# Kernel optimization log

Hardware: AMD Instinct MI355X
Metric: run time of the kernel (lower is better)

## Reference

```python
import math
import jax, jax.numpy as jnp
import numpy as np

NUM_HEADS, RAD_PTS, LVL_PTS = 8, 4, 1
P = RAD_PTS * LVL_PTS


def setup_inputs() -> dict:
    B, Nq, Din = 2, 21760, 256
    hw = np.array([[128, 128], [64, 64], [32, 32], [16, 16]], np.int64)
    sizes = hw[:, 0] * hw[:, 1]
    offs = np.concatenate([[0], np.cumsum(sizes)[:-1]]).astype(np.int64)
    Ns = int(sizes.sum())
    map_ids = np.tile(np.repeat(np.arange(4), sizes)[None], (B, 1)).astype(np.int64)

    key = jax.random.key(0)
    ks = jax.random.split(key, 8)
    in_feats = jax.random.normal(ks[0], (B, Nq, Din), jnp.float32)
    sample_feats = jax.random.normal(ks[1], (B, Ns, Din), jnp.float32)
    sample_priors = jax.random.uniform(ks[2], (B, Nq, 2), jnp.float32)

    # sample_offsets bias: radial grid init as in the torch module
    thetas = np.arange(NUM_HEADS) * (2.0 * math.pi / NUM_HEADS)
    grid = np.stack([np.cos(thetas), np.sin(thetas), np.zeros(NUM_HEADS)], 1)
    grid = grid / np.abs(grid).max(1, keepdims=True)
    grid = np.tile(grid.reshape(NUM_HEADS, 1, 1, 3), (1, RAD_PTS, LVL_PTS, 1))
    grid = grid * np.arange(1, RAD_PTS + 1).reshape(1, RAD_PTS, 1, 1)
    bo = jnp.asarray(grid.reshape(-1), jnp.float32)

    Wo = jax.random.normal(ks[3], (NUM_HEADS * P * 3, Din), jnp.float32) * 0.01
    Wa = jax.random.normal(ks[4], (NUM_HEADS * P, Din), jnp.float32) * 0.01
    ba = jnp.zeros((NUM_HEADS * P,), jnp.float32)
    s = 1.0 / np.sqrt(Din)
    Wv = jax.random.normal(ks[5], (Din, Din), jnp.float32) * s
    bv = jnp.zeros((Din,), jnp.float32)
    Wout = jax.random.normal(ks[6], (Din, Din), jnp.float32) * s
    bout = jnp.zeros((Din,), jnp.float32)

    return dict(in_feats=in_feats, sample_priors=sample_priors, sample_feats=sample_feats,
                map_hw=jnp.asarray(hw), map_offs=jnp.asarray(offs), map_ids=jnp.asarray(map_ids),
                Wo=Wo, bo=bo, Wa=Wa, ba=ba, Wv=Wv, bv=bv, Wout=Wout, bout=bout)


def _trilinear_sample(val, map_hw, map_offs, xy, z, L):
    # val [B,Ns,H,D]; xy [B,Q,H,P,2] normalized; z [B,Q,H,P] in ~[0,1]
    B, Ns, H, D = val.shape
    Q = xy.shape[1]
    val_t = val.transpose(0, 2, 1, 3)  # [B,H,Ns,D]
    x, y = xy[..., 0], xy[..., 1]
    lvl_f = z * (L - 1)
    l0 = jnp.floor(lvl_f).astype(jnp.int32)
    wz = lvl_f - l0.astype(lvl_f.dtype)

    def gather(idx):  # idx [B,Q,H,P] int32 -> [B,Q,H,P,D]
        it = idx.transpose(0, 2, 1, 3).reshape(B, H, Q * P, 1)
        g = jnp.take_along_axis(val_t, it, axis=2)  # [B,H,Q*P,D]
        return g.reshape(B, H, Q, P, D).transpose(0, 2, 1, 3, 4)

    def sample_level(lvl):  # bilinear sample within pyramid level `lvl` (zero padding)
        valid_l = (lvl >= 0) & (lvl < L)
        lc = jnp.clip(lvl, 0, L - 1)
        Hl = map_hw[lc, 0].astype(jnp.int32)
        Wl = map_hw[lc, 1].astype(jnp.int32)
        off = map_offs[lc].astype(jnp.int32)
        xf = x * Wl.astype(x.dtype) - 0.5
        yf = y * Hl.astype(x.dtype) - 0.5
        x0 = jnp.floor(xf).astype(jnp.int32)
        y0 = jnp.floor(yf).astype(jnp.int32)
        dx = xf - x0.astype(x.dtype)
        dy = yf - y0.astype(x.dtype)
        out = jnp.zeros((B, Q, H, P, D), x.dtype)
        corners = [(x0, y0, (1 - dx) * (1 - dy)), (x0 + 1, y0, dx * (1 - dy)),
                   (x0, y0 + 1, (1 - dx) * dy), (x0 + 1, y0 + 1, dx * dy)]
        for xi, yi, w in corners:
            ok = valid_l & (xi >= 0) & (xi < Wl) & (yi >= 0) & (yi < Hl)
            idx = off + jnp.clip(yi, 0, Hl - 1) * Wl + jnp.clip(xi, 0, Wl - 1)
            out = out + gather(idx) * (w * ok.astype(x.dtype))[..., None]
        return out

    return sample_level(l0) * (1 - wz)[..., None] + sample_level(l0 + 1) * wz[..., None]


def reference(in_feats, sample_priors, sample_feats, map_hw, map_offs, map_ids,
              Wo, bo, Wa, ba, Wv, bv, Wout, bout):
    B, Nq, _ = in_feats.shape
    Ns = sample_feats.shape[1]
    L = map_hw.shape[0]
    D = Wv.shape[0] // NUM_HEADS

    val = (sample_feats @ Wv.T + bv).reshape(B, Ns, NUM_HEADS, D)
    offs = (in_feats @ Wo.T + bo).reshape(B, Nq, NUM_HEADS, P, 3)

    # sample_priors last dim == 2: normalize offsets by (W, H) of the query's map
    norm = map_hw[:, ::-1][map_ids].astype(offs.dtype)  # [B,Nq,2] (w,h)
    sample_xy = sample_priors[:, :, None, None, :2] + offs[..., :2] / norm[:, :, None, None, :]

    lvl_off = jnp.arange(LVL_PTS, dtype=offs.dtype) - 0.5 * (LVL_PTS - 1)
    z_grid = map_ids[:, :, None, None, None].astype(offs.dtype) + lvl_off  # [B,Nq,1,1,Lp]
    z_grid = jnp.broadcast_to(z_grid, (B, Nq, NUM_HEADS, RAD_PTS, LVL_PTS)).reshape(B, Nq, NUM_HEADS, P)
    sample_z = (z_grid + jnp.tanh(offs[..., 2])) / (L - 1)

    attn = jax.nn.softmax((in_feats @ Wa.T + ba).reshape(B, Nq, NUM_HEADS, P), axis=3)

    sampled = _trilinear_sample(val, map_hw, map_offs, sample_xy, sample_z, L)  # [B,Nq,H,P,D]
    attn_feats = jnp.einsum('bqhpd,bqhp->bqhd', sampled, attn).reshape(B, Nq, NUM_HEADS * D)
    return attn_feats @ Wout.T + bout
```

## Files before the change

### kernel.cpp

```cpp
#include <hip/hip_runtime.h>
#include <hip/hip_bf16.h>
#include <math.h>

typedef __bf16 bf16x8 __attribute__((ext_vector_type(8)));
typedef float f32x4 __attribute__((ext_vector_type(4)));
typedef float f32x2 __attribute__((ext_vector_type(2)));
typedef unsigned short ushort8 __attribute__((ext_vector_type(8)));

static __device__ __forceinline__ unsigned short f2bf(float f) {
    union { float f; unsigned u; } c; c.f = f;
    unsigned r = c.u + 0x7FFFu + ((c.u >> 16) & 1u);
    return (unsigned short)(r >> 16);
}

static __device__ __forceinline__ void gload_lds16(
    const unsigned short* g, unsigned short* l)
{
    __builtin_amdgcn_global_load_lds(
        (const __attribute__((address_space(1))) void*)g,
        (__attribute__((address_space(3))) void*)l, 16, 0, 0);
}

__global__ __launch_bounds__(256) void convert_weights_hist(
    const float* __restrict__ Wv, const float* __restrict__ Wo,
    const float* __restrict__ Wa, const float* __restrict__ Wout,
    const float* __restrict__ bo, const float* __restrict__ ba,
    unsigned short* __restrict__ Wv_b, unsigned short* __restrict__ Woa_b,
    unsigned short* __restrict__ Wout_b, float* __restrict__ boa,
    const float* __restrict__ priors, int* __restrict__ counts,
    int BQ, int Nq)
{
    __shared__ int cnt[16];
    if (threadIdx.x < 16) cnt[threadIdx.x] = 0;
    __syncthreads();

    int gid = blockIdx.x * blockDim.x + threadIdx.x;
    int stride = gridDim.x * blockDim.x;
    for (int i = gid; i < 163840; i += stride) {
        if (i < 65536)       Wv_b[i] = f2bf(Wv[i]);
        else if (i < 90112)  Woa_b[i - 65536] = f2bf(Wo[i - 65536]);
        else if (i < 98304)  Woa_b[i - 65536] = f2bf(Wa[i - 90112]);
        else                 Wout_b[i - 98304] = f2bf(Wout[i - 98304]);
    }
    if (gid < 96)       boa[gid] = bo[gid];
    else if (gid < 128) boa[gid] = ba[gid - 96];

    for (int q = gid; q < BQ; q += stride) {
        int b = q / Nq;
        float py = priors[(size_t)q * 2 + 1];
        int band = min(7, max(0, (int)(py * 8.0f)));
        atomicAdd(&cnt[b * 8 + band], 1);
    }
    __syncthreads();
    if (threadIdx.x < 16 && cnt[threadIdx.x] > 0)
        atomicAdd(&counts[threadIdx.x], cnt[threadIdx.x]);
}

__global__ __launch_bounds__(256) void bucket_scatter(
    const float* __restrict__ priors, const int* __restrict__ counts,
    int* __restrict__ cursors, int* __restrict__ qidx, int BQ, int Nq)
{
    __shared__ int lcnt[16];
    __shared__ int lbase[16];
    const int tid = threadIdx.x;
    if (tid < 16) lcnt[tid] = 0;
    __syncthreads();
    int q = blockIdx.x * 256 + tid;
    int mybucket = 0, myslot = 0;
    bool valid = q < BQ;
    if (valid) {
        int b = q / Nq;
        float py = priors[(size_t)q * 2 + 1];
        int band = min(7, max(0, (int)(py * 8.0f)));
        mybucket = b * 8 + band;
        myslot = atomicAdd(&lcnt[mybucket], 1);
    }
    __syncthreads();
    if (tid < 16) {
        int base = 0;
        #pragma unroll
        for (int i = 0; i < 16; ++i) base += (i < tid) ? counts[i] : 0;
        lbase[tid] = base + atomicAdd(&cursors[tid], lcnt[tid]);
    }
    __syncthreads();
    if (valid) qidx[lbase[mybucket] + myslot] = q;
}

template<int WN, bool A_BF16, int OUT_MODE>
__global__ __launch_bounds__(WN * 64) void gemm_mfma(
    const void* __restrict__ Av, const unsigned short* __restrict__ W,
    const float* __restrict__ bias, void* __restrict__ Cv,
    int M, int N, int K, int NsPB)
{
    constexpr int BM = 64;
    constexpr int BN = WN * 64;
    constexpr int BK = 64;
    constexpr int NTHR = WN * 64;
    constexpr int LDP = 72;
    constexpr int ASZ = A_BF16 ? (BM * 64) : (BM * LDP);

    __shared__ __align__(16) unsigned short As[ASZ];
    __shared__ __align__(16) unsigned short Bs[BN * 64];

    const int bm  = blockIdx.x * BM;
    const int bn  = blockIdx.y * BN;
    const int tid = threadIdx.x;
    const int wid = tid >> 6;
    const int lane = tid & 63;
    const int lr = lane & 15;
    const int lg = lane >> 4;
    const int lrow = lane >> 3;
    const int lc16 = (lane & 7) ^ (lrow & 7);

    f32x4 acc[4][4];
    #pragma unroll
    for (int mi = 0; mi < 4; ++mi)
        #pragma unroll
        for (int ni = 0; ni < 4; ++ni)
            acc[mi][ni] = (f32x4){0.f, 0.f, 0.f, 0.f};

    for (int kt = 0; kt < K; kt += BK) {
        #pragma unroll
        for (int c = wid; c < BN / 8; c += WN) {
            const unsigned short* g =
                W + (size_t)(bn + c * 8 + lrow) * K + kt + lc16 * 8;
            gload_lds16(g, Bs + c * 512);
        }
        if (A_BF16) {
            const unsigned short* A = (const unsigned short*)Av;
            #pragma unroll
            for (int c = wid; c < BM / 8; c += WN) {
                const unsigned short* g =
                    A + (size_t)(bm + c * 8 + lrow) * K + kt + lc16 * 8;
                gload_lds16(g, As + c * 512);
            }
        } else {
            const float* A = (const float*)Av;
            #pragma unroll
            for (int u = tid; u < BM * 8; u += NTHR) {
                int r = u >> 3, kb = u & 7;
                const float* src = A + (size_t)(bm + r) * K + kt + kb * 8;
                float4 f0 = *(const float4*)(src);
                float4 f1 = *(const float4*)(src + 4);
                ushort8 v;
                v[0] = f2bf(f0.x); v[1] = f2bf(f0.y);
                v[2] = f2bf(f0.z); v[3] = f2bf(f0.w);
                v[4] = f2bf(f1.x); v[5] = f2bf(f1.y);
                v[6] = f2bf(f1.z); v[7] = f2bf(f1.w);
                *(ushort8*)(As + r * LDP + kb * 8) = v;
            }
        }
        __syncthreads();

        #pragma unroll
        for (int kk = 0; kk < 2; ++kk) {
            bf16x8 fa[4], fb[4];
            #pragma unroll
            for (int mi = 0; mi < 4; ++mi) {
                if (A_BF16) {
                    int row = mi * 16 + lr;
                    fa[mi] = *(const bf16x8*)(As + row * 64 +
                                              ((kk * 4 + lg) ^ (lr & 7)) * 8);
                } else {
                    fa[mi] = *(const bf16x8*)(As + (mi * 16 + lr) * LDP +
                                              kk * 32 + lg * 8);
                }
            }
            #pragma unroll
            for (int ni = 0; ni < 4; ++ni) {
                int row = wid * 64 + ni * 16 + lr;
                fb[ni] = *(const bf16x8*)(Bs + row * 64 +
                                          ((kk * 4 + lg) ^ (lr & 7)) * 8);
            }
            #pragma unroll
            for (int mi = 0; mi < 4; ++mi)
                #pragma unroll
                for (int ni = 0; ni < 4; ++ni)
                    acc[mi][ni] = __builtin_amdgcn_mfma_f32_16x16x32_bf16(
                        fa[mi], fb[ni], acc[mi][ni], 0, 0, 0);
        }
        __syncthreads();
    }

    if (OUT_MODE == 2) {
        const int b = bm / NsPB;
        const int ns_base = bm - b * NsPB;
        #pragma unroll
        for (int ni = 0; ni < 4; ++ni) {
            int col = wid * 64 + ni * 16 + lr;
            int h   = col >> 5;
            int ch  = col & 31;
            float bv = bias[col];
            unsigned short* dst = (unsigned short*)Cv +
                (size_t)(b * 8 + h) * NsPB * 32 + ch;
            #pragma unroll
            for (int mi = 0; mi < 4; ++mi) {
                #pragma unroll
                for (int r = 0; r < 4; ++r) {
                    int ns = ns_base + mi * 16 + lg * 4 + r;
                    dst[(size_t)ns * 32] = f2bf(acc[mi][ni][r] + bv);
                }
            }
        }
    } else {
        #pragma unroll
        for (int ni = 0; ni < 4; ++ni) {
            int col = bn + wid * 64 + ni * 16 + lr;
            float bv = bias[col];
            #pragma unroll
            for (int mi = 0; mi < 4; ++mi) {
                #pragma unroll
                for (int r = 0; r < 4; ++r) {
                    int row = bm + mi * 16 + lg * 4 + r;
                    if (OUT_MODE == 1) {
                        ((unsigned short*)Cv)[(size_t)row * N + col] =
                            f2bf(acc[mi][ni][r] + bv);
                    } else {
                        ((float*)Cv)[(size_t)row * N + col] = acc[mi][ni][r] + bv;
                    }
                }
            }
        }
    }
}

__global__ __launch_bounds__(256) void msda_sample_kernel(
    const float* __restrict__ C1,
    const float* __restrict__ priors,
    const unsigned short* __restrict__ val,
    const int*   __restrict__ map_hw,
    const int*   __restrict__ map_offs,
    const int*   __restrict__ map_ids,
    const int*   __restrict__ qidx,
    unsigned short* __restrict__ out,
    int Nq, int Ns)
{
    const int swz  = (blockIdx.x & 7) * (gridDim.x >> 3) + (blockIdx.x >> 3);
    const int wvi  = threadIdx.x >> 6;
    const int lane = threadIdx.x & 63;
    const int bq   = qidx[swz * 4 + wvi];
    const int b    = bq / Nq;
    const int q    = bq - b * Nq;

    __shared__ __align__(16) float s_rec[4][4][128];

    {
        const int hp = lane >> 1;
        const int sl = lane & 1;
        const float* sc = C1 + (size_t)bq * 128;
        float o0 = sc[hp * 3 + 0];
        float o1 = sc[hp * 3 + 1];
        float o2 = sc[hp * 3 + 2];
        float logit = sc[96 + hp];

        float m = logit;
        m = fmaxf(m, __shfl_xor(m, 2));
        m = fmaxf(m, __shfl_xor(m, 4));
        float e = expf(logit - m);
        float s = e;
        s += __shfl_xor(s, 2);
        s += __shfl_xor(s, 4);
        float attnw = e / s;

        int lid = map_ids[(size_t)b * Ns + q];
        float px = priors[(size_t)bq * 2 + 0];
        float py = priors[(size_t)bq * 2 + 1];
        int Hq = map_hw[lid * 2 + 0];
        int Wq = map_hw[lid * 2 + 1];
        float x = px + o0 / (float)Wq;
        float y = py + o1 / (float)Hq;

        float lvl_f = (float)lid + tanhf(o2);
        float l0f = floorf(lvl_f);
        int   l0  = (int)l0f;
        float wz  = lvl_f - l0f;

        const int   lv = l0 + sl;
        const float wl = sl ? wz : (1.0f - wz);
        float w4[4];
        int   i4[4];
        if (lv >= 0 && lv < 4) {
            int Hs  = map_hw[lv * 2 + 0];
            int Ws  = map_hw[lv * 2 + 1];
            int off = map_offs[lv];
            float xf = x * (float)Ws - 0.5f;
            float yf = y * (float)Hs - 0.5f;
            float x0f = floorf(xf), y0f = floorf(yf);
            int   x0  = (int)x0f,  y0  = (int)y0f;
            float dx = xf - x0f, dy = yf - y0f;
            #pragma unroll
            for (int j = 0; j < 4; ++j) {
                int xi = x0 + (j & 1);
                int yi = y0 + (j >> 1);
                float w = ((j & 1) ? dx : 1.0f - dx) *
                          ((j >> 1) ? dy : 1.0f - dy);
                bool ok = (xi >= 0) && (xi < Ws) && (yi >= 0) && (yi < Hs);
                w4[j] = ok ? (w * wl * attnw) : 0.0f;
                i4[j] = ok ? ((off + yi * Ws + xi) << 6) : 0;
            }
        } else {
            #pragma unroll
            for (int j = 0; j < 4; ++j) { w4[j] = 0.0f; i4[j] = 0; }
        }
        f32x4 wrec = {w4[0], w4[1], w4[2], w4[3]};
        f32x4 irec = {__int_as_float(i4[0]), __int_as_float(i4[1]),
                      __int_as_float(i4[2]), __int_as_float(i4[3])};
        *(f32x4*)&s_rec[wvi][sl][hp * 4]     = wrec;
        *(f32x4*)&s_rec[wvi][2 + sl][hp * 4] = irec;
    }
    asm volatile("s_waitcnt lgkmcnt(0)" ::: "memory");

    const int p2 = lane & 1;
    const int d8 = (lane >> 1) & 3;
    const int h  = lane >> 3;
    const char* vbase = (const char*)(val + (size_t)(b * 8 + h) * Ns * 32)
                        + d8 * 16;

    f32x2 acc2[4];
    #pragma unroll
    for (int k = 0; k < 4; ++k) acc2[k] = (f32x2){0.f, 0.f};

    #pragma unroll
    for (int pp = 0; pp < 2; ++pp) {
        const int hp = h * 4 + p2 + pp * 2;
        f32x4 wlo = *(const f32x4*)&s_rec[wvi][0][hp * 4];
        f32x4 whi = *(const f32x4*)&s_rec[wvi][1][hp * 4];
        f32x4 xlo = *(const f32x4*)&s_rec[wvi][2][hp * 4];
        f32x4 xhi = *(const f32x4*)&s_rec[wvi][3][hp * 4];

        uint4 u[8];
        #pragma unroll
        for (int j = 0; j < 4; ++j)
            u[j] = *(const uint4*)(vbase + __float_as_int(xlo[j]));
        #pragma unroll
        for (int j = 0; j < 4; ++j)
            u[4 + j] = *(const uint4*)(vbase + __float_as_int(xhi[j]));

        #pragma unroll
        for (int j = 0; j < 8; ++j) {
            float w = (j < 4) ? wlo[j] : whi[j - 4];
            f32x2 w2 = {w, w};
            unsigned ua[4] = {u[j].x, u[j].y, u[j].z, u[j].w};
            #pragma unroll
            for (int k = 0; k < 4; ++k) {
                union { unsigned u; float f; } lo, hi;
                lo.u = ua[k] << 16;
                hi.u = ua[k] & 0xffff0000u;
                f32x2 v2 = {lo.f, hi.f};
                acc2[k] += w2 * v2;
            }
        }
    }

    #pragma unroll
    for (int k = 0; k < 4; ++k) {
        acc2[k][0] += __shfl_xor(acc2[k][0], 1);
        acc2[k][1] += __shfl_xor(acc2[k][1], 1);
    }

    if (p2 == 0) {
        ushort8 o;
        #pragma unroll
        for (int k = 0; k < 4; ++k) {
            o[2 * k]     = f2bf(acc2[k][0]);
            o[2 * k + 1] = f2bf(acc2[k][1]);
        }
        *(ushort8*)(out + (size_t)bq * 256 + h * 32 + d8 * 8) = o;
    }
}

extern "C" void kernel_launch(void* const* d_in, const int* in_sizes, int n_in,
                              void* d_out, int out_size, void* d_ws, size_t ws_size,
                              hipStream_t stream) {
    const float* in_feats      = (const float*)d_in[0];
    const float* sample_priors = (const float*)d_in[1];
    const float* sample_feats  = (const float*)d_in[2];
    const int*   map_hw        = (const int*)d_in[3];
    const int*   map_offs      = (const int*)d_in[4];
    const int*   map_ids       = (const int*)d_in[5];
    const float* Wo            = (const float*)d_in[6];
    const float* bo            = (const float*)d_in[7];
    const float* Wa            = (const float*)d_in[8];
    const float* ba            = (const float*)d_in[9];
    const float* Wv            = (const float*)d_in[10];
    const float* bv            = (const float*)d_in[11];
    const float* Wout          = (const float*)d_in[12];
    const float* bout          = (const float*)d_in[13];
    float* out = (float*)d_out;

    const int B = 2, Nq = 21760, Din = 256;
    const int Ns = in_sizes[2] / (B * Din);
    const int BQ = B * Nq;

    unsigned short* val = (unsigned short*)d_out;
    float* C1 = (float*)d_ws;
    unsigned short* af = (unsigned short*)((char*)d_ws + (size_t)BQ * 128 * 4);
    char* wbase = (char*)d_ws + (size_t)BQ * 128 * 4 + (size_t)BQ * 256 * 2;
    unsigned short* Wv_b   = (unsigned short*)wbase;
    unsigned short* Woa_b  = Wv_b + 65536;
    unsigned short* Wout_b = Woa_b + 32768;
    float* boa = (float*)(Wout_b + 65536);
    int* bws  = (int*)(boa + 128);
    int* qidx = bws + 32;

    hipMemsetAsync(bws, 0, 128, stream);

    convert_weights_hist<<<dim3(160), dim3(256), 0, stream>>>(
        Wv, Wo, Wa, Wout, bo, ba, Wv_b, Woa_b, Wout_b, boa,
        sample_priors, bws, BQ, Nq);

    bucket_scatter<<<dim3((BQ + 255) / 256), dim3(256), 0, stream>>>(
        sample_priors, bws, bws + 16, qidx, BQ, Nq);

    gemm_mfma<4, false, 2><<<dim3(BQ / 64, 1), dim3(256), 0, stream>>>(
        sample_feats, Wv_b, bv, val, B * Ns, 256, Din, Ns);

    gemm_mfma<2, false, 0><<<dim3(BQ / 64, 1), dim3(128), 0, stream>>>(
        in_feats, Woa_b, boa, C1, BQ, 128, Din, Ns);

    msda_sample_kernel<<<dim3(BQ / 4), dim3(256), 0, stream>>>(
        C1, sample_priors, val, map_hw, map_offs, map_ids, qidx, af, Nq, Ns);

    gemm_mfma<4, true, 0><<<dim3(BQ / 64, 1), dim3(256), 0, stream>>>(
        af, Wout_b, bout, out, BQ, 256, Din, Ns);
}
```

Measured before the change: 108.4 us.

## Store offset/attention logits as bf16, widen GEMM tile, batch sampler gathers

```diff
diff --git a/kernel.cpp b/kernel.cpp
--- a/kernel.cpp
+++ b/kernel.cpp
@@ -11,6 +11,10 @@
     union { float f; unsigned u; } c; c.f = f;
     unsigned r = c.u + 0x7FFFu + ((c.u >> 16) & 1u);
     return (unsigned short)(r >> 16);
+}
+static __device__ __forceinline__ float bf2f(unsigned short u) {
+    union { unsigned u; float f; } c; c.u = ((unsigned)u) << 16;
+    return c.f;
 }
 
 static __device__ __forceinline__ void gload_lds16(
@@ -86,16 +90,17 @@
     if (valid) qidx[lbase[mybucket] + myslot] = q;
 }
 
-template<int WN, bool A_BF16, int OUT_MODE>
-__global__ __launch_bounds__(WN * 64) void gemm_mfma(
+template<int WM, int WN, bool A_BF16, int OUT_MODE>
+__global__ __launch_bounds__(WM * WN * 64) void gemm_mfma(
     const void* __restrict__ Av, const unsigned short* __restrict__ W,
     const float* __restrict__ bias, void* __restrict__ Cv,
     int M, int N, int K, int NsPB)
 {
-    constexpr int BM = 64;
+    constexpr int BM = WM * 64;
     constexpr int BN = WN * 64;
     constexpr int BK = 64;
-    constexpr int NTHR = WN * 64;
+    constexpr int NWAVE = WM * WN;
+    constexpr int NTHR = NWAVE * 64;
     constexpr int LDP = 72;
     constexpr int ASZ = A_BF16 ? (BM * 64) : (BM * LDP);
 
@@ -106,6 +111,8 @@
     const int bn  = blockIdx.y * BN;
     const int tid = threadIdx.x;
     const int wid = tid >> 6;
+    const int wrow = wid / WN;
+    const int wcol = wid % WN;
     const int lane = tid & 63;
     const int lr = lane & 15;
     const int lg = lane >> 4;
@@ -121,7 +128,7 @@
 
     for (int kt = 0; kt < K; kt += BK) {
         #pragma unroll
-        for (int c = wid; c < BN / 8; c += WN) {
+        for (int c = wid; c < BN / 8; c += NWAVE) {
             const unsigned short* g =
                 W + (size_t)(bn + c * 8 + lrow) * K + kt + lc16 * 8;
             gload_lds16(g, Bs + c * 512);
@@ -129,7 +136,7 @@
         if (A_BF16) {
             const unsigned short* A = (const unsigned short*)Av;
             #pragma unroll
-            for (int c = wid; c < BM / 8; c += WN) {
+            for (int c = wid; c < BM / 8; c += NWAVE) {
                 const unsigned short* g =
                     A + (size_t)(bm + c * 8 + lrow) * K + kt + lc16 * 8;
                 gload_lds16(g, As + c * 512);
@@ -157,18 +164,18 @@
             bf16x8 fa[4], fb[4];
             #pragma unroll
             for (int mi = 0; mi < 4; ++mi) {
+                int row = wrow * 64 + mi * 16 + lr;
                 if (A_BF16) {
-                    int row = mi * 16 + lr;
                     fa[mi] = *(const bf16x8*)(As + row * 64 +
                                               ((kk * 4 + lg) ^ (lr & 7)) * 8);
                 } else {
-                    fa[mi] = *(const bf16x8*)(As + (mi * 16 + lr) * LDP +
+                    fa[mi] = *(const bf16x8*)(As + row * LDP +
                                               kk * 32 + lg * 8);
                 }
             }
             #pragma unroll
             for (int ni = 0; ni < 4; ++ni) {
-                int row = wid * 64 + ni * 16 + lr;
+                int row = wcol * 64 + ni * 16 + lr;
                 fb[ni] = *(const bf16x8*)(Bs + row * 64 +
                                           ((kk * 4 + lg) ^ (lr & 7)) * 8);
             }
@@ -187,7 +194,7 @@
         const int ns_base = bm - b * NsPB;
         #pragma unroll
         for (int ni = 0; ni < 4; ++ni) {
-            int col = wid * 64 + ni * 16 + lr;
+            int col = wcol * 64 + ni * 16 + lr;
             int h   = col >> 5;
             int ch  = col & 31;
             float bv = bias[col];
@@ -205,13 +212,13 @@
     } else {
         #pragma unroll
         for (int ni = 0; ni < 4; ++ni) {
-            int col = bn + wid * 64 + ni * 16 + lr;
+            int col = bn + wcol * 64 + ni * 16 + lr;
             float bv = bias[col];
             #pragma unroll
             for (int mi = 0; mi < 4; ++mi) {
                 #pragma unroll
                 for (int r = 0; r < 4; ++r) {
-                    int row = bm + mi * 16 + lg * 4 + r;
+                    int row = bm + wrow * 64 + mi * 16 + lg * 4 + r;
                     if (OUT_MODE == 1) {
                         ((unsigned short*)Cv)[(size_t)row * N + col] =
                             f2bf(acc[mi][ni][r] + bv);
@@ -225,7 +232,7 @@
 }
 
 __global__ __launch_bounds__(256) void msda_sample_kernel(
-    const float* __restrict__ C1,
+    const unsigned short* __restrict__ C1,
     const float* __restrict__ priors,
     const unsigned short* __restrict__ val,
     const int*   __restrict__ map_hw,
@@ -247,11 +254,11 @@
     {
         const int hp = lane >> 1;
         const int sl = lane & 1;
-        const float* sc = C1 + (size_t)bq * 128;
-        float o0 = sc[hp * 3 + 0];
-        float o1 = sc[hp * 3 + 1];
-        float o2 = sc[hp * 3 + 2];
-        float logit = sc[96 + hp];
+        const unsigned short* sc = C1 + (size_t)bq * 128;
+        float o0 = bf2f(sc[hp * 3 + 0]);
+        float o1 = bf2f(sc[hp * 3 + 1]);
+        float o2 = bf2f(sc[hp * 3 + 2]);
+        float logit = bf2f(sc[96 + hp]);
 
         float m = logit;
         m = fmaxf(m, __shfl_xor(m, 2));
@@ -316,31 +323,35 @@
     const char* vbase = (const char*)(val + (size_t)(b * 8 + h) * Ns * 32)
                         + d8 * 16;
 
-    f32x2 acc2[4];
-    #pragma unroll
-    for (int k = 0; k < 4; ++k) acc2[k] = (f32x2){0.f, 0.f};
-
+    f32x4 wrec[4], irec[4];
     #pragma unroll
     for (int pp = 0; pp < 2; ++pp) {
         const int hp = h * 4 + p2 + pp * 2;
-        f32x4 wlo = *(const f32x4*)&s_rec[wvi][0][hp * 4];
-        f32x4 whi = *(const f32x4*)&s_rec[wvi][1][hp * 4];
-        f32x4 xlo = *(const f32x4*)&s_rec[wvi][2][hp * 4];
-        f32x4 xhi = *(const f32x4*)&s_rec[wvi][3][hp * 4];
-
-        uint4 u[8];
+        wrec[pp * 2 + 0] = *(const f32x4*)&s_rec[wvi][0][hp * 4];
+        wrec[pp * 2 + 1] = *(const f32x4*)&s_rec[wvi][1][hp * 4];
+        irec[pp * 2 + 0] = *(const f32x4*)&s_rec[wvi][2][hp * 4];
+        irec[pp * 2 + 1] = *(const f32x4*)&s_rec[wvi][3][hp * 4];
+    }
+
+    uint4 u[16];
+    #pragma unroll
+    for (int r = 0; r < 4; ++r)
         #pragma unroll
         for (int j = 0; j < 4; ++j)
-            u[j] = *(const uint4*)(vbase + __float_as_int(xlo[j]));
-        #pragma unroll
-        for (int j = 0; j < 4; ++j)
-            u[4 + j] = *(const uint4*)(vbase + __float_as_int(xhi[j]));
-
-        #pragma unroll
-        for (int j = 0; j < 8; ++j) {
-            float w = (j < 4) ? wlo[j] : whi[j - 4];
+            u[r * 4 + j] = *(const uint4*)(vbase + __float_as_int(irec[r][j]));
+
+    f32x2 acc2[4];
+    #pragma unroll
+    for (int k = 0; k < 4; ++k) acc2[k] = (f32x2){0.f, 0.f};
+
+    #pragma unroll
+    for (int r = 0; r < 4; ++r) {
+        #pragma unroll
+        for (int j = 0; j < 4; ++j) {
+            float w = wrec[r][j];
             f32x2 w2 = {w, w};
-            unsigned ua[4] = {u[j].x, u[j].y, u[j].z, u[j].w};
+            unsigned ua[4] = {u[r * 4 + j].x, u[r * 4 + j].y,
+                              u[r * 4 + j].z, u[r * 4 + j].w};
             #pragma unroll
             for (int k = 0; k < 4; ++k) {
                 union { unsigned u; float f; } lo, hi;
@@ -393,9 +404,9 @@
     const int BQ = B * Nq;
 
     unsigned short* val = (unsigned short*)d_out;
-    float* C1 = (float*)d_ws;
-    unsigned short* af = (unsigned short*)((char*)d_ws + (size_t)BQ * 128 * 4);
-    char* wbase = (char*)d_ws + (size_t)BQ * 128 * 4 + (size_t)BQ * 256 * 2;
+    unsigned short* C1b = (unsigned short*)d_ws;
+    unsigned short* af  = C1b + (size_t)BQ * 128;
+    char* wbase = (char*)(af + (size_t)BQ * 256);
     unsigned short* Wv_b   = (unsigned short*)wbase;
     unsigned short* Woa_b  = Wv_b + 65536;
     unsigned short* Wout_b = Woa_b + 32768;
@@ -412,15 +423,15 @@
     bucket_scatter<<<dim3((BQ + 255) / 256), dim3(256), 0, stream>>>(
         sample_priors, bws, bws + 16, qidx, BQ, Nq);
 
-    gemm_mfma<4, false, 2><<<dim3(BQ / 64, 1), dim3(256), 0, stream>>>(
+    gemm_mfma<1, 4, false, 2><<<dim3(BQ / 64, 1), dim3(256), 0, stream>>>(
         sample_feats, Wv_b, bv, val, B * Ns, 256, Din, Ns);
 
-    gemm_mfma<2, false, 0><<<dim3(BQ / 64, 1), dim3(128), 0, stream>>>(
-        in_feats, Woa_b, boa, C1, BQ, 128, Din, Ns);
+    gemm_mfma<2, 2, false, 1><<<dim3(BQ / 128, 1), dim3(256), 0, stream>>>(
+        in_feats, Woa_b, boa, C1b, BQ, 128, Din, Ns);
 
     msda_sample_kernel<<<dim3(BQ / 4), dim3(256), 0, stream>>>(
-        C1, sample_priors, val, map_hw, map_offs, map_ids, qidx, af, Nq, Ns);
-
-    gemm_mfma<4, true, 0><<<dim3(BQ / 64, 1), dim3(256), 0, stream>>>(
+        C1b, sample_priors, val, map_hw, map_offs, map_ids, qidx, af, Nq, Ns);
+
+    gemm_mfma<1, 4, true, 0><<<dim3(BQ / 64, 1), dim3(256), 0, stream>>>(
         af, Wout_b, bout, out, BQ, 256, Din, Ns);
 }
```

New measurement: 114.9 us. +6.1%, slower.
